# Kernel tuning notes

Hardware: AMD Instinct MI355X
Metric: run time of the kernel (lower is better)

The kernel has to match this reference:

```python
import jax, jax.numpy as jnp
import numpy as np

H = 16
D_MODEL = 1024
BLOCK_SIZE = 64
B, S = 2, 2048
NEG = -65504.0  # value used by the torch module for masking


def setup_inputs() -> dict:
    key = jax.random.key(0)
    ks = jax.random.split(key, 12)
    scale = 1.0 / np.sqrt(D_MODEL)
    inp = {
        "query": jax.random.normal(ks[0], (B, S, D_MODEL), jnp.float32),
        "key": jax.random.normal(ks[1], (B, S, D_MODEL), jnp.float32),
        "value": jax.random.normal(ks[2], (B, S, D_MODEL), jnp.float32),
        "Wq": jax.random.normal(ks[3], (D_MODEL, D_MODEL), jnp.float32) * scale,
        "bq": jnp.zeros((D_MODEL,), jnp.float32),
        "Wk": jax.random.normal(ks[4], (D_MODEL, D_MODEL), jnp.float32) * scale,
        "bk": jnp.zeros((D_MODEL,), jnp.float32),
        "Wv": jax.random.normal(ks[5], (D_MODEL, D_MODEL), jnp.float32) * scale,
        "bv": jnp.zeros((D_MODEL,), jnp.float32),
        "Wo": jax.random.normal(ks[6], (D_MODEL, D_MODEL), jnp.float32) * scale,
        "bo": jnp.zeros((D_MODEL,), jnp.float32),
    }
    return inp


def reference(query, key, value, Wq, bq, Wk, bk, Wv, bv, Wo, bo):
    b, s, d = query.shape
    dk = d // H

    def proj(x, W, bias):
        # [b,s,d] -> [b,h,s,dk]
        return (x @ W + bias).reshape(b, s, H, dk).transpose(0, 2, 1, 3)

    q = proj(query, Wq, bq)
    k = proj(key, Wk, bk)
    v = proj(value, Wv, bv)

    # dense QK^T / sqrt(d_k), exactly as the torch module (then block mask added)
    scores = jnp.einsum("bhqd,bhkd->bhqk", q, k) / jnp.sqrt(jnp.float32(dk))

    bid = jnp.arange(s) // BLOCK_SIZE
    attn_mask = jnp.where(bid[:, None] == bid[None, :], 0.0, NEG).astype(scores.dtype)
    scores = scores + attn_mask  # broadcast over [b,h]

    attn = jax.nn.softmax(scores, axis=-1)
    x = jnp.einsum("bhqk,bhkd->bhqd", attn, v)
    x = x.transpose(0, 2, 1, 3).reshape(b, s, d)
    return x @ Wo + bo
```

## Files before the change

kernel.cpp:

```cpp
#include <hip/hip_runtime.h>
#include <hip/hip_bf16.h>

typedef __attribute__((ext_vector_type(4))) float f32x4;
typedef __attribute__((ext_vector_type(8))) short s16x8;

#define MFMA16(a, b, c) __builtin_amdgcn_mfma_f32_16x16x32_bf16(a, b, c, 0, 0, 0)

__device__ __forceinline__ void gld_lds16(const void* g, void* l) {
  __builtin_amdgcn_global_load_lds(
      (const __attribute__((address_space(1))) unsigned int*)g,
      (__attribute__((address_space(3))) unsigned int*)l, 16, 0, 0);
}

__device__ __forceinline__ unsigned short f2bf(float f) {
  union { __hip_bfloat16 b; unsigned short u; } cv;
  cv.b = __float2bfloat16(f);
  return cv.u;
}
__device__ __forceinline__ float bf2f(unsigned short u) {
  union { unsigned short u; __hip_bfloat16 b; } cv;
  cv.u = u;
  return __bfloat162float(cv.b);
}

__global__ void transw(const float* W0, unsigned short* H0,
                       const float* W1, unsigned short* H1,
                       const float* W2, unsigned short* H2,
                       const float* W3, unsigned short* H3) {
  __shared__ float tile[64 * 65];
  const float* W; unsigned short* H;
  switch (blockIdx.y) {
    case 0: W = W0; H = H0; break;
    case 1: W = W1; H = H1; break;
    case 2: W = W2; H = H2; break;
    default: W = W3; H = H3; break;
  }
  const int t = threadIdx.x;
  const int tk0 = (blockIdx.x & 15) * 64;
  const int tn0 = (blockIdx.x >> 4) * 64;
  for (int i = 0; i < 16; ++i) {
    int idx = i * 256 + t;
    int r = idx >> 6, c = idx & 63;
    tile[r * 65 + c] = W[(size_t)(tk0 + r) * 1024 + tn0 + c];
  }
  __syncthreads();
  for (int i = 0; i < 16; ++i) {
    int idx = i * 256 + t;
    int r = idx >> 6, c = idx & 63;
    H[(size_t)(tn0 + r) * 1024 + tk0 + c] = f2bf(tile[c * 65 + r]);
  }
}

__global__ void convert_x3(const float* A0, unsigned short* H0,
                           const float* A1, unsigned short* H1,
                           const float* A2, unsigned short* H2) {
  const float* src; unsigned short* h;
  switch (blockIdx.y) {
    case 0: src = A0; h = H0; break;
    case 1: src = A1; h = H1; break;
    default: src = A2; h = H2; break;
  }
  int i = blockIdx.x * 256 + threadIdx.x;
  float4 v = ((const float4*)src)[i];
  ((ushort4*)h)[i] = make_ushort4(f2bf(v.x), f2bf(v.y), f2bf(v.z), f2bf(v.w));
}

struct QkvArgs {
  const unsigned short* A[3];
  const unsigned short* B[3];
  const float* bias[3];
  unsigned short* out[3];
};

__global__ __launch_bounds__(512, 2)
void gemm_qkv(QkvArgs args) {
  const int K = 1024;
  __shared__ __align__(16) unsigned short lds[4][2][8192];
  const int tid = threadIdx.x;
  const int lane = tid & 63, w = tid >> 6;

  const int nwg = 192;
  const int orig = blockIdx.x;
  const int swz = (orig & 7) * (nwg >> 3) + (orig >> 3);
  const int g = swz >> 6;
  const int tl = swz & 63;
  const int m0 = (tl >> 2) * 256, n0 = (tl & 3) * 256;

  const unsigned short* A = args.A[g];
  const unsigned short* B = args.B[g];
  const float* bias = args.bias[g];
  unsigned short* out = args.out[g];

  const int wm = (w >> 2) * 128, wn = (w & 3) * 64;
  const int fr = lane & 15, gh = lane >> 4;

  size_t aoff[2], boff[2]; int dst[2];
  #pragma unroll
  for (int i = 0; i < 2; ++i) {
    const int G = i * 512 + tid;
    const int rp = G >> 3, spr = G & 7;
    const int s = spr ^ (rp & 7);
    const int srow = 2 * rp + (s >> 2), ko = (s & 3) * 8;
    aoff[i] = (size_t)(m0 + srow) * K + ko;
    boff[i] = (size_t)(n0 + srow) * K + ko;
    dst[i] = G * 8;
  }

  auto stage = [&](int buf, int kt) {
    gld_lds16(A + aoff[0] + kt, &lds[buf][0][dst[0]]);
    gld_lds16(A + aoff[1] + kt, &lds[buf][0][dst[1]]);
    gld_lds16(B + boff[0] + kt, &lds[buf][1][dst[0]]);
    gld_lds16(B + boff[1] + kt, &lds[buf][1][dst[1]]);
  };

  f32x4 acc[8][4] = {};
  const int laneoff = (fr >> 1) * 64 + ((((fr & 1) << 2) | gh) ^ (fr >> 1)) * 8;

  stage(0, 0); stage(1, 32); stage(2, 64);
  asm volatile("s_waitcnt vmcnt(8)" ::: "memory");
  __builtin_amdgcn_s_barrier();
  __builtin_amdgcn_sched_barrier(0);

  #pragma unroll 1
  for (int t = 0; t < 32; ++t) {
    const int buf = t & 3;
    const unsigned short* La = &lds[buf][0][wm * 32 + laneoff];
    const unsigned short* Lb = &lds[buf][1][wn * 32 + laneoff];
    s16x8 a[8], b[4];
    #pragma unroll
    for (int nt = 0; nt < 4; ++nt) b[nt] = *(const s16x8*)&Lb[nt * 512];
    #pragma unroll
    for (int mt = 0; mt < 8; ++mt) a[mt] = *(const s16x8*)&La[mt * 512];
    if (t <= 28) stage((t + 3) & 3, (t + 3) * 32);
    __builtin_amdgcn_s_setprio(1);
    #pragma unroll
    for (int mt = 0; mt < 8; ++mt)
      #pragma unroll
      for (int nt = 0; nt < 4; ++nt)
        acc[mt][nt] = MFMA16(a[mt], b[nt], acc[mt][nt]);
    __builtin_amdgcn_s_setprio(0);
    if (t < 29)       { asm volatile("s_waitcnt vmcnt(8)" ::: "memory"); }
    else if (t == 29) { asm volatile("s_waitcnt vmcnt(4)" ::: "memory"); }
    else if (t == 30) { asm volatile("s_waitcnt vmcnt(0)" ::: "memory"); }
    __builtin_amdgcn_s_barrier();
    __builtin_amdgcn_sched_barrier(0);
  }

  float bv[4];
  #pragma unroll
  for (int nt = 0; nt < 4; ++nt) bv[nt] = bias[n0 + wn + nt * 16 + fr];
  unsigned short* eb = &lds[0][0][0];
  __syncthreads();
  if (g == 2) {
    #pragma unroll
    for (int mt = 0; mt < 8; ++mt)
      #pragma unroll
      for (int nt = 0; nt < 4; ++nt) {
        const int nl = wn + nt * 16 + fr;
        f32x4 r = acc[mt][nt];
        #pragma unroll
        for (int j = 0; j < 4; ++j) {
          const int sl = wm + mt * 16 + gh * 4 + j;
          eb[sl * 256 + (nl ^ ((sl >> 3) & 31))] = f2bf(r[j] + bv[nt]);
        }
      }
  } else {
    #pragma unroll
    for (int mt = 0; mt < 8; ++mt)
      #pragma unroll
      for (int nt = 0; nt < 4; ++nt) {
        const int nl = wn + nt * 16 + fr;
        f32x4 r = acc[mt][nt];
        #pragma unroll
        for (int j = 0; j < 4; ++j) {
          const int sl = wm + mt * 16 + gh * 4 + j;
          eb[sl * 256 + nl] = f2bf(r[j] + bv[nt]);
        }
      }
  }
  __syncthreads();
  const int b2 = m0 >> 11;
  if (g == 2) {
    #pragma unroll
    for (int it = 0; it < 16; ++it) {
      const int u = it * 512 + tid;
      const int nl = u >> 5, sc = u & 31;
      s16x8 v;
      #pragma unroll
      for (int r = 0; r < 8; ++r)
        v[r] = (short)eb[(sc * 8 + r) * 256 + (nl ^ sc)];
      const int gn = n0 + nl, h = gn >> 6, d = gn & 63;
      *(s16x8*)&out[((size_t)((b2 * 16 + h) * 64 + d)) * 2048 + (m0 & 2047) + sc * 8] = v;
    }
  } else {
    #pragma unroll
    for (int it = 0; it < 16; ++it) {
      const int u = it * 512 + tid;
      const int sl = u >> 5, n8 = (u & 31) * 8;
      s16x8 v = *(const s16x8*)&eb[sl * 256 + n8];
      const int s = m0 + sl;
      const int gn = n0 + n8, h = gn >> 6, d = gn & 63;
      *(s16x8*)&out[(((size_t)(b2 * 16 + h)) * 2048 + (s & 2047)) * 64 + d] = v;
    }
  }
}

__global__ __launch_bounds__(256, 3)
void gemm_oproj(const unsigned short* __restrict__ A, const unsigned short* __restrict__ B,
                const float* __restrict__ bias, float* __restrict__ out) {
  const int K = 1024, N = 1024;
  __shared__ __align__(16) unsigned short lds[3][2][4096];
  const int tid = threadIdx.x;
  const int lane = tid & 63, wid = tid >> 6;

  const int nwg = 256;
  const int orig = blockIdx.x;
  const int swz = (orig & 7) * (nwg >> 3) + (orig >> 3);
  const int m0 = (swz >> 3) * 128, n0 = (swz & 7) * 128;

  const int wm = (wid >> 1) * 64, wn = (wid & 1) * 64;
  const int fr = lane & 15, gh = lane >> 4;

  size_t aoff[2], boff[2]; int dst[2];
  #pragma unroll
  for (int i = 0; i < 2; ++i) {
    const int G = i * 256 + tid;
    const int rp = G >> 3, spr = G & 7;
    const int s = spr ^ (rp & 7);
    const int srow = 2 * rp + (s >> 2), ko = (s & 3) * 8;
    aoff[i] = (size_t)(m0 + srow) * K + ko;
    boff[i] = (size_t)(n0 + srow) * K + ko;
    dst[i] = G * 8;
  }

  auto stage = [&](int buf, int kt) {
    #pragma unroll
    for (int i = 0; i < 2; ++i) {
      gld_lds16(A + aoff[i] + kt, &lds[buf][0][dst[i]]);
      gld_lds16(B + boff[i] + kt, &lds[buf][1][dst[i]]);
    }
  };

  f32x4 acc[4][4] = {};
  const int laneoff = (fr >> 1) * 64 + ((((fr & 1) << 2) | gh) ^ (fr >> 1)) * 8;

  stage(0, 0); stage(1, 32);
  asm volatile("s_waitcnt vmcnt(4)" ::: "memory");
  __builtin_amdgcn_s_barrier();
  __builtin_amdgcn_sched_barrier(0);

  #pragma unroll 1
  for (int t = 0; t < 32; ++t) {
    const int buf = t % 3;
    const unsigned short* La = &lds[buf][0][wm * 32 + laneoff];
    const unsigned short* Lb = &lds[buf][1][wn * 32 + laneoff];
    s16x8 b[4], a[4];
    #pragma unroll
    for (int nt = 0; nt < 4; ++nt) b[nt] = *(const s16x8*)&Lb[nt * 512];
    #pragma unroll
    for (int mt = 0; mt < 4; ++mt) a[mt] = *(const s16x8*)&La[mt * 512];
    if (t <= 29) stage((t + 2) % 3, (t + 2) * 32);
    __builtin_amdgcn_s_setprio(1);
    #pragma unroll
    for (int mt = 0; mt < 4; ++mt)
      #pragma unroll
      for (int nt = 0; nt < 4; ++nt)
        acc[mt][nt] = MFMA16(a[mt], b[nt], acc[mt][nt]);
    __builtin_amdgcn_s_setprio(0);
    if (t < 30)       { asm volatile("s_waitcnt vmcnt(4)" ::: "memory"); }
    else if (t == 30) { asm volatile("s_waitcnt vmcnt(0)" ::: "memory"); }
    __builtin_amdgcn_s_barrier();
    __builtin_amdgcn_sched_barrier(0);
  }

  #pragma unroll
  for (int mt = 0; mt < 4; ++mt) {
    const int gm = m0 + wm + mt * 16 + (gh << 2);
    #pragma unroll
    for (int nt = 0; nt < 4; ++nt) {
      const int gn = n0 + wn + nt * 16 + fr;
      const float bvv = bias[gn];
      f32x4 r = acc[mt][nt];
      #pragma unroll
      for (int j = 0; j < 4; ++j)
        out[(size_t)(gm + j) * N + gn] = r[j] + bvv;
    }
  }
}

__global__ __launch_bounds__(256, 2)
void attn_mfma(const unsigned short* __restrict__ Q, const unsigned short* __restrict__ Kb,
               const unsigned short* __restrict__ Vt, unsigned short* __restrict__ X) {
  __shared__ __align__(16) unsigned short qs[4096];
  __shared__ __align__(16) unsigned short ks2[4096];
  __shared__ __align__(16) unsigned short vs[4096];
  __shared__ __align__(16) unsigned short ps[4096];
  const int tid = threadIdx.x, lane = tid & 63, w = tid >> 6;
  const int hb = blockIdx.x >> 5, qb = blockIdx.x & 31;
  const size_t qkbase = ((size_t)hb * 2048 + qb * 64) * 64;
  const size_t vbase = (size_t)hb * 64 * 2048 + qb * 64;

  #pragma unroll
  for (int i = 0; i < 2; ++i) {
    const int G = i * 256 + tid;
    const int row = G >> 3, slot = G & 7;
    const int sg = slot ^ (row & 7);
    gld_lds16(Q + qkbase + row * 64 + sg * 8, &qs[G * 8]);
    gld_lds16(Kb + qkbase + row * 64 + sg * 8, &ks2[G * 8]);
    gld_lds16(Vt + vbase + (size_t)row * 2048 + sg * 8, &vs[G * 8]);
  }
  asm volatile("s_waitcnt vmcnt(0)" ::: "memory");
  __syncthreads();

  const int fr = lane & 15, gh = lane >> 4;
  const int arow = w * 16 + fr;

  s16x8 aq[2], bk[2][4];
  #pragma unroll
  for (int ks = 0; ks < 2; ++ks) {
    aq[ks] = *(const s16x8*)&qs[arow * 64 + (((ks * 4 + gh) ^ (arow & 7)) << 3)];
    #pragma unroll
    for (int nt = 0; nt < 4; ++nt) {
      const int krow = nt * 16 + fr;
      bk[ks][nt] = *(const s16x8*)&ks2[krow * 64 + (((ks * 4 + gh) ^ (krow & 7)) << 3)];
    }
  }
  f32x4 s[4] = {};
  #pragma unroll
  for (int ks = 0; ks < 2; ++ks)
    #pragma unroll
    for (int nt = 0; nt < 4; ++nt)
      s[nt] = MFMA16(aq[ks], bk[ks][nt], s[nt]);

  #pragma unroll
  for (int j = 0; j < 4; ++j) {
    float t0 = s[0][j] * 0.125f, t1 = s[1][j] * 0.125f;
    float t2 = s[2][j] * 0.125f, t3 = s[3][j] * 0.125f;
    float m = fmaxf(fmaxf(t0, t1), fmaxf(t2, t3));
    m = fmaxf(m, __shfl_xor(m, 1, 64));
    m = fmaxf(m, __shfl_xor(m, 2, 64));
    m = fmaxf(m, __shfl_xor(m, 4, 64));
    m = fmaxf(m, __shfl_xor(m, 8, 64));
    t0 = __expf(t0 - m); t1 = __expf(t1 - m);
    t2 = __expf(t2 - m); t3 = __expf(t3 - m);
    float sum = t0 + t1 + t2 + t3;
    sum += __shfl_xor(sum, 1, 64);
    sum += __shfl_xor(sum, 2, 64);
    sum += __shfl_xor(sum, 4, 64);
    sum += __shfl_xor(sum, 8, 64);
    const float r = 1.0f / sum;
    s[0][j] = t0 * r; s[1][j] = t1 * r; s[2][j] = t2 * r; s[3][j] = t3 * r;
  }

  #pragma unroll
  for (int j = 0; j < 4; ++j) {
    const int q = w * 16 + gh * 4 + j;
    #pragma unroll
    for (int nt = 0; nt < 4; ++nt) {
      const int k = nt * 16 + fr;
      ps[q * 64 + (((k >> 3) ^ (q & 7)) << 3) + (k & 7)] = f2bf(s[nt][j]);
    }
  }

  s16x8 ap[2], bv2[2][4];
  #pragma unroll
  for (int ks = 0; ks < 2; ++ks) {
    ap[ks] = *(const s16x8*)&ps[arow * 64 + (((ks * 4 + gh) ^ (arow & 7)) << 3)];
    #pragma unroll
    for (int nt = 0; nt < 4; ++nt) {
      const int drow = nt * 16 + fr;
      bv2[ks][nt] = *(const s16x8*)&vs[drow * 64 + (((ks * 4 + gh) ^ (drow & 7)) << 3)];
    }
  }
  f32x4 x[4] = {};
  #pragma unroll
  for (int ks = 0; ks < 2; ++ks)
    #pragma unroll
    for (int nt = 0; nt < 4; ++nt)
      x[nt] = MFMA16(ap[ks], bv2[ks][nt], x[nt]);

  const int b = hb >> 4, h = hb & 15;
  #pragma unroll
  for (int nt = 0; nt < 4; ++nt)
    #pragma unroll
    for (int j = 0; j < 4; ++j) {
      const int sgl = qb * 64 + w * 16 + gh * 4 + j;
      X[((size_t)(b * 2048 + sgl)) * 1024 + h * 64 + nt * 16 + fr] = f2bf(x[nt][j]);
    }
}

extern "C" void kernel_launch(void* const* d_in, const int* in_sizes, int n_in,
                              void* d_out, int out_size, void* d_ws, size_t ws_size,
                              hipStream_t stream) {
  const float* query = (const float*)d_in[0];
  const float* key   = (const float*)d_in[1];
  const float* value = (const float*)d_in[2];
  const float* Wq = (const float*)d_in[3]; const float* bq = (const float*)d_in[4];
  const float* Wk = (const float*)d_in[5]; const float* bk = (const float*)d_in[6];
  const float* Wv = (const float*)d_in[7]; const float* bv = (const float*)d_in[8];
  const float* Wo = (const float*)d_in[9]; const float* bo = (const float*)d_in[10];
  float* out = (float*)d_out;

  const size_t W_E = 1024 * 1024;
  const size_t X_E = 4096 * 1024;
  unsigned char* p = (unsigned char*)d_ws;
  auto take = [&](size_t bytes) { void* r = (void*)p; p += bytes; return r; };

  unsigned short* wtq = (unsigned short*)take(W_E * 2);
  unsigned short* wtk = (unsigned short*)take(W_E * 2);
  unsigned short* wtv = (unsigned short*)take(W_E * 2);
  unsigned short* wto = (unsigned short*)take(W_E * 2);
  unsigned short* xq = (unsigned short*)take(X_E * 2);
  unsigned short* xk = (unsigned short*)take(X_E * 2);
  unsigned short* xv = (unsigned short*)take(X_E * 2);
  unsigned short* Qb = (unsigned short*)take(X_E * 2);
  unsigned short* Kb = (unsigned short*)take(X_E * 2);
  unsigned short* Vt = (unsigned short*)take(X_E * 2);
  unsigned short* ao = (unsigned short*)take(X_E * 2);
  (void)ws_size; (void)in_sizes; (void)n_in; (void)out_size;

  transw<<<dim3(256, 4), 256, 0, stream>>>(Wq, wtq, Wk, wtk, Wv, wtv, Wo, wto);
  convert_x3<<<dim3(4096, 3), 256, 0, stream>>>(query, xq, key, xk, value, xv);

  QkvArgs qkv = {};
  qkv.A[0] = xq; qkv.B[0] = wtq; qkv.bias[0] = bq; qkv.out[0] = Qb;
  qkv.A[1] = xk; qkv.B[1] = wtk; qkv.bias[1] = bk; qkv.out[1] = Kb;
  qkv.A[2] = xv; qkv.B[2] = wtv; qkv.bias[2] = bv; qkv.out[2] = Vt;
  gemm_qkv<<<dim3(192), 512, 0, stream>>>(qkv);

  attn_mfma<<<dim3(1024), 256, 0, stream>>>(Qb, Kb, Vt, ao);

  gemm_oproj<<<dim3(256), 256, 0, stream>>>(ao, wto, bo, out);
}
```

Measured before the change: 79.79 us.

## Switch QKV and output GEMMs to double-buffered K=64 tiles with interleaved A loads

Both GEMM kernels move from a 3–4 stage pipeline with K=32 tiles to a 2-stage double buffer with K=64 tiles and a new XOR-swizzled LDS layout. Each iteration now loads A fragments in chunks interleaved with MFMAs, which cuts loop iterations and barriers by half. The trade-off is a shallower prefetch (wait vmcnt(0) every iteration) and, for the output projection, larger LDS use, so its occupancy hint drops from 3 to 2. The risk is more exposed memory latency.

```diff
diff --git a/kernel.cpp b/kernel.cpp
--- a/kernel.cpp
+++ b/kernel.cpp
@@ -65,6 +65,7 @@
   ((ushort4*)h)[i] = make_ushort4(f2bf(v.x), f2bf(v.y), f2bf(v.z), f2bf(v.w));
 }
 
+
 struct QkvArgs {
   const unsigned short* A[3];
   const unsigned short* B[3];
@@ -75,7 +76,7 @@
 __global__ __launch_bounds__(512, 2)
 void gemm_qkv(QkvArgs args) {
   const int K = 1024;
-  __shared__ __align__(16) unsigned short lds[4][2][8192];
+  __shared__ __align__(16) unsigned short lds[65536];
   const int tid = threadIdx.x;
   const int lane = tid & 63, w = tid >> 6;
 
@@ -94,54 +95,66 @@
   const int wm = (w >> 2) * 128, wn = (w & 3) * 64;
   const int fr = lane & 15, gh = lane >> 4;
 
-  size_t aoff[2], boff[2]; int dst[2];
-  #pragma unroll
-  for (int i = 0; i < 2; ++i) {
-    const int G = i * 512 + tid;
-    const int rp = G >> 3, spr = G & 7;
-    const int s = spr ^ (rp & 7);
-    const int srow = 2 * rp + (s >> 2), ko = (s & 3) * 8;
-    aoff[i] = (size_t)(m0 + srow) * K + ko;
-    boff[i] = (size_t)(n0 + srow) * K + ko;
-    dst[i] = G * 8;
-  }
-
-  auto stage = [&](int buf, int kt) {
-    gld_lds16(A + aoff[0] + kt, &lds[buf][0][dst[0]]);
-    gld_lds16(A + aoff[1] + kt, &lds[buf][0][dst[1]]);
-    gld_lds16(B + boff[0] + kt, &lds[buf][1][dst[0]]);
-    gld_lds16(B + boff[1] + kt, &lds[buf][1][dst[1]]);
+  const unsigned short* aP[4]; const unsigned short* bP[4]; int dstoff[4];
+  #pragma unroll
+  for (int s = 0; s < 4; ++s) {
+    const int G = s * 512 + tid;
+    const int r = G >> 3, slot = G & 7;
+    const int gno = slot ^ (r & 7);
+    const int ko = (gno >> 2) * 32 + (gno & 3) * 8;
+    aP[s] = A + (size_t)(m0 + r) * K + ko;
+    bP[s] = B + (size_t)(n0 + r) * K + ko;
+    dstoff[s] = G * 8;
+  }
+  auto stageAll = [&](int u, int kt) {
+    #pragma unroll
+    for (int s = 0; s < 4; ++s) {
+      gld_lds16(aP[s] + kt, &lds[u * 16384 + dstoff[s]]);
+      gld_lds16(bP[s] + kt, &lds[32768 + u * 16384 + dstoff[s]]);
+    }
   };
 
   f32x4 acc[8][4] = {};
-  const int laneoff = (fr >> 1) * 64 + ((((fr & 1) << 2) | gh) ^ (fr >> 1)) * 8;
-
-  stage(0, 0); stage(1, 32); stage(2, 64);
-  asm volatile("s_waitcnt vmcnt(8)" ::: "memory");
+
+  stageAll(0, 0);
+  asm volatile("s_waitcnt vmcnt(0)" ::: "memory");
   __builtin_amdgcn_s_barrier();
   __builtin_amdgcn_sched_barrier(0);
 
   #pragma unroll 1
-  for (int t = 0; t < 32; ++t) {
-    const int buf = t & 3;
-    const unsigned short* La = &lds[buf][0][wm * 32 + laneoff];
-    const unsigned short* Lb = &lds[buf][1][wn * 32 + laneoff];
-    s16x8 a[8], b[4];
-    #pragma unroll
-    for (int nt = 0; nt < 4; ++nt) b[nt] = *(const s16x8*)&Lb[nt * 512];
-    #pragma unroll
-    for (int mt = 0; mt < 8; ++mt) a[mt] = *(const s16x8*)&La[mt * 512];
-    if (t <= 28) stage((t + 3) & 3, (t + 3) * 32);
-    __builtin_amdgcn_s_setprio(1);
-    #pragma unroll
-    for (int mt = 0; mt < 8; ++mt)
-      #pragma unroll
-      for (int nt = 0; nt < 4; ++nt)
-        acc[mt][nt] = MFMA16(a[mt], b[nt], acc[mt][nt]);
-    __builtin_amdgcn_s_setprio(0);
-    if (t < 29)       { asm volatile("s_waitcnt vmcnt(8)" ::: "memory"); }
-    else if (t == 29) { asm volatile("s_waitcnt vmcnt(4)" ::: "memory"); }
-    else if (t == 30) { asm volatile("s_waitcnt vmcnt(0)" ::: "memory"); }
+  for (int t = 0; t < 16; ++t) {
+    const int u = t & 1;
+    if (t < 15) stageAll(u ^ 1, (t + 1) * 64);
+    const unsigned short* La = &lds[u * 16384];
+    const unsigned short* Lb = &lds[32768 + u * 16384];
+    s16x8 b[2][4];
+    #pragma unroll
+    for (int ks = 0; ks < 2; ++ks)
+      #pragma unroll
+      for (int nt = 0; nt < 4; ++nt) {
+        const int br = wn + nt * 16 + fr;
+        b[ks][nt] = *(const s16x8*)&Lb[br * 64 + (((ks << 2) | gh) ^ (br & 7)) * 8];
+      }
+    #pragma unroll
+    for (int q = 0; q < 4; ++q) {
+      s16x8 a[2][2];
+      #pragma unroll
+      for (int i = 0; i < 2; ++i)
+        #pragma unroll
+        for (int ks = 0; ks < 2; ++ks) {
+          const int ar = wm + (q * 2 + i) * 16 + fr;
+          a[i][ks] = *(const s16x8*)&La[ar * 64 + (((ks << 2) | gh) ^ (ar & 7)) * 8];
+        }
+      #pragma unroll
+      for (int i = 0; i < 2; ++i)
+        #pragma unroll
+        for (int nt = 0; nt < 4; ++nt) {
+          acc[q * 2 + i][nt] = MFMA16(a[i][0], b[0][nt], acc[q * 2 + i][nt]);
+          acc[q * 2 + i][nt] = MFMA16(a[i][1], b[1][nt], acc[q * 2 + i][nt]);
+        }
+    }
+    __builtin_amdgcn_sched_barrier(0);
+    if (t < 15) { asm volatile("s_waitcnt vmcnt(0)" ::: "memory"); }
     __builtin_amdgcn_s_barrier();
     __builtin_amdgcn_sched_barrier(0);
   }
@@ -149,7 +162,7 @@
   float bv[4];
   #pragma unroll
   for (int nt = 0; nt < 4; ++nt) bv[nt] = bias[n0 + wn + nt * 16 + fr];
-  unsigned short* eb = &lds[0][0][0];
+  unsigned short* eb = &lds[0];
   __syncthreads();
   if (g == 2) {
     #pragma unroll
@@ -205,11 +218,11 @@
   }
 }
 
-__global__ __launch_bounds__(256, 3)
+__global__ __launch_bounds__(256, 2)
 void gemm_oproj(const unsigned short* __restrict__ A, const unsigned short* __restrict__ B,
                 const float* __restrict__ bias, float* __restrict__ out) {
   const int K = 1024, N = 1024;
-  __shared__ __align__(16) unsigned short lds[3][2][4096];
+  __shared__ __align__(16) unsigned short lds[32768];
   const int tid = threadIdx.x;
   const int lane = tid & 63, wid = tid >> 6;
 
@@ -221,54 +234,66 @@
   const int wm = (wid >> 1) * 64, wn = (wid & 1) * 64;
   const int fr = lane & 15, gh = lane >> 4;
 
-  size_t aoff[2], boff[2]; int dst[2];
-  #pragma unroll
-  for (int i = 0; i < 2; ++i) {
-    const int G = i * 256 + tid;
-    const int rp = G >> 3, spr = G & 7;
-    const int s = spr ^ (rp & 7);
-    const int srow = 2 * rp + (s >> 2), ko = (s & 3) * 8;
-    aoff[i] = (size_t)(m0 + srow) * K + ko;
-    boff[i] = (size_t)(n0 + srow) * K + ko;
-    dst[i] = G * 8;
-  }
-
-  auto stage = [&](int buf, int kt) {
-    #pragma unroll
-    for (int i = 0; i < 2; ++i) {
-      gld_lds16(A + aoff[i] + kt, &lds[buf][0][dst[i]]);
-      gld_lds16(B + boff[i] + kt, &lds[buf][1][dst[i]]);
+  const unsigned short* aP[4]; const unsigned short* bP[4]; int dstoff[4];
+  #pragma unroll
+  for (int s = 0; s < 4; ++s) {
+    const int G = s * 256 + tid;
+    const int r = G >> 3, slot = G & 7;
+    const int gno = slot ^ (r & 7);
+    const int ko = (gno >> 2) * 32 + (gno & 3) * 8;
+    aP[s] = A + (size_t)(m0 + r) * K + ko;
+    bP[s] = B + (size_t)(n0 + r) * K + ko;
+    dstoff[s] = G * 8;
+  }
+  auto stageAll = [&](int u, int kt) {
+    #pragma unroll
+    for (int s = 0; s < 4; ++s) {
+      gld_lds16(aP[s] + kt, &lds[u * 8192 + dstoff[s]]);
+      gld_lds16(bP[s] + kt, &lds[16384 + u * 8192 + dstoff[s]]);
     }
   };
 
   f32x4 acc[4][4] = {};
-  const int laneoff = (fr >> 1) * 64 + ((((fr & 1) << 2) | gh) ^ (fr >> 1)) * 8;
-
-  stage(0, 0); stage(1, 32);
-  asm volatile("s_waitcnt vmcnt(4)" ::: "memory");
+
+  stageAll(0, 0);
+  asm volatile("s_waitcnt vmcnt(0)" ::: "memory");
   __builtin_amdgcn_s_barrier();
   __builtin_amdgcn_sched_barrier(0);
 
   #pragma unroll 1
-  for (int t = 0; t < 32; ++t) {
-    const int buf = t % 3;
-    const unsigned short* La = &lds[buf][0][wm * 32 + laneoff];
-    const unsigned short* Lb = &lds[buf][1][wn * 32 + laneoff];
-    s16x8 b[4], a[4];
-    #pragma unroll
-    for (int nt = 0; nt < 4; ++nt) b[nt] = *(const s16x8*)&Lb[nt * 512];
-    #pragma unroll
-    for (int mt = 0; mt < 4; ++mt) a[mt] = *(const s16x8*)&La[mt * 512];
-    if (t <= 29) stage((t + 2) % 3, (t + 2) * 32);
-    __builtin_amdgcn_s_setprio(1);
-    #pragma unroll
-    for (int mt = 0; mt < 4; ++mt)
-      #pragma unroll
-      for (int nt = 0; nt < 4; ++nt)
-        acc[mt][nt] = MFMA16(a[mt], b[nt], acc[mt][nt]);
-    __builtin_amdgcn_s_setprio(0);
-    if (t < 30)       { asm volatile("s_waitcnt vmcnt(4)" ::: "memory"); }
-    else if (t == 30) { asm volatile("s_waitcnt vmcnt(0)" ::: "memory"); }
+  for (int t = 0; t < 16; ++t) {
+    const int u = t & 1;
+    if (t < 15) stageAll(u ^ 1, (t + 1) * 64);
+    const unsigned short* La = &lds[u * 8192];
+    const unsigned short* Lb = &lds[16384 + u * 8192];
+    s16x8 b[2][4];
+    #pragma unroll
+    for (int ks = 0; ks < 2; ++ks)
+      #pragma unroll
+      for (int nt = 0; nt < 4; ++nt) {
+        const int br = wn + nt * 16 + fr;
+        b[ks][nt] = *(const s16x8*)&Lb[br * 64 + (((ks << 2) | gh) ^ (br & 7)) * 8];
+      }
+    #pragma unroll
+    for (int q = 0; q < 2; ++q) {
+      s16x8 a[2][2];
+      #pragma unroll
+      for (int i = 0; i < 2; ++i)
+        #pragma unroll
+        for (int ks = 0; ks < 2; ++ks) {
+          const int ar = wm + (q * 2 + i) * 16 + fr;
+          a[i][ks] = *(const s16x8*)&La[ar * 64 + (((ks << 2) | gh) ^ (ar & 7)) * 8];
+        }
+      #pragma unroll
+      for (int i = 0; i < 2; ++i)
+        #pragma unroll
+        for (int nt = 0; nt < 4; ++nt) {
+          acc[q * 2 + i][nt] = MFMA16(a[i][0], b[0][nt], acc[q * 2 + i][nt]);
+          acc[q * 2 + i][nt] = MFMA16(a[i][1], b[1][nt], acc[q * 2 + i][nt]);
+        }
+    }
+    __builtin_amdgcn_sched_barrier(0);
+    if (t < 15) { asm volatile("s_waitcnt vmcnt(0)" ::: "memory"); }
     __builtin_amdgcn_s_barrier();
     __builtin_amdgcn_sched_barrier(0);
   }
```

Measured after the change: 78.93 us. Within noise of the previous version (-1.1%).
